# Kernel tuning notes

Hardware: AMD Instinct MI355X
Metric: run time of the kernel (lower is better)

Reference implementation:

```python
import jax, jax.numpy as jnp
import numpy as np

KERNEL_SIZE = (3, 3)
STRIDE = 1
PADDING = 'valid'  # 'valid' -> no padding; 'same' -> pad per module's pad_tensor


def setup_inputs() -> dict:
    key = jax.random.key(0)
    kx, kk = jax.random.split(key)
    C_in, H, W = 16, 2048, 2048
    C_out = 16
    hf, wf = KERNEL_SIZE
    x = jax.random.normal(kx, (C_in, H, W), dtype=jnp.float32)
    kernels = jax.random.normal(kk, (C_out, C_in, hf, wf), dtype=jnp.float32)
    return {"x": x, "kernels": kernels}


def _conv(x, kernels):
    # x: (C,H,W); kernels: (C_out,C_in,hf,wf)
    # The torch module's im2col + mm is exactly a cross-correlation (no kernel
    # flip), i.e., standard conv in DL convention.
    if PADDING == 'same':
        hf, wf = KERNEL_SIZE
        ph, pw = (hf - 1) // 2, (wf - 1) // 2
        # NOTE: original ConstantPad3d((0,0,pad_h,pad_h,pad_w,pad_w)) pads H by
        # pad_h and C by pad_w on a (C,H,W) tensor; for square kernels with
        # hf==wf the intended symmetric spatial pad is equivalent here.
        x = jnp.pad(x, ((0, 0), (ph, ph), (pw, pw)))
    out = jax.lax.conv_general_dilated(
        x[None],                      # (1,C,H,W)
        kernels,                      # (O,I,hf,wf)
        window_strides=(STRIDE, STRIDE),
        padding='VALID',
        dimension_numbers=('NCHW', 'OIHW', 'NCHW'),
    )
    return out[0]                     # (C_out,H_out,W_out)


def reference(x, kernels):
    return _conv(x, kernels)
```

## Files before the change

kernel.cpp:

```cpp
#include <hip/hip_runtime.h>


#define HIN   2048
#define WIN   2048
#define HOUT  2046
#define WOUT  2046
#define PLANE_IN  (HIN * WIN)
#define PLANE_OUT (HOUT * WOUT)
#define TR 34
#define TC 36
#define NTASK (TR * 18 * 2)
#define WF_U32 (5 * 64 * 4)

typedef __attribute__((ext_vector_type(8))) short bf16x8;
typedef __attribute__((ext_vector_type(4))) float f32x4;
typedef __attribute__((ext_vector_type(4))) unsigned u32x4;
typedef f32x4 __attribute__((aligned(4))) f32x4_u;

static __device__ __forceinline__ short f2bf(float f) {
    unsigned u = __float_as_uint(f);
    return (short)((u + 0x7FFFu + ((u >> 16) & 1u)) >> 16);
}
static __device__ __forceinline__ unsigned pk2(float lo, float hi) {
    unsigned a = __float_as_uint(lo);
    unsigned b = __float_as_uint(hi);
    a = (a + 0x7FFFu + ((a >> 16) & 1u)) >> 16;
    b = (b + 0x7FFFu + ((b >> 16) & 1u)) & 0xFFFF0000u;
    return a | b;
}

__global__ __launch_bounds__(64)
void wf_setup(const float* __restrict__ k, unsigned* __restrict__ wfbuf) {
    int lane = threadIdx.x;
    int m = lane & 15, g = lane >> 4;
    #pragma unroll
    for (int i = 0; i < 5; ++i) {
        u32x4 q;
        #pragma unroll
        for (int jj = 0; jj < 4; ++jj) {
            unsigned r = 0;
            #pragma unroll
            for (int e = 0; e < 2; ++e) {
                int kk  = 32 * i + 8 * g + 2 * jj + e;
                int tap = kk >> 4;
                int ci  = kk & 15;
                unsigned v = 0;
                if (tap < 9) v = (unsigned short)f2bf(k[(m * 16 + ci) * 9 + tap]);
                r |= v << (16 * e);
            }
            q[jj] = r;
        }
        *(u32x4*)(wfbuf + (i * 64 + lane) * 4) = q;
    }
}

__global__ __launch_bounds__(512, 6)
void conv3x3_fused(const float* __restrict__ x,
                   const unsigned* __restrict__ wfbuf,
                   float* __restrict__ out) {
    __shared__ unsigned lds[TR * TC * 8];

    const int tid  = threadIdx.x;
    const int lane = tid & 63;
    const int wv   = tid >> 6;
    const int m    = lane & 15;
    const int g    = lane >> 4;

    int bid = blockIdx.x;
    int swz = (bid & 7) * 512 + (bid >> 3);
    int h0 = (swz >> 6) * 32; if (h0 > HOUT - 32) h0 = HOUT - 32;
    int w0 = (swz & 63) * 32;

    #pragma unroll
    for (int p = 0; p < 3; ++p) {
        int t = p * 512 + tid;
        if (t < NTASK) {
            int wp  = t % 18;
            int r2  = t / 18;
            int cih = r2 & 1;
            int row = r2 >> 1;
            int c   = 2 * wp;
            int w   = w0 + c; if (w > WIN - 2) w = WIN - 2;
            const float* gp = x + (size_t)(cih * 8) * PLANE_IN
                                + (size_t)(h0 + row) * WIN + w;
            float2 f0 = *(const float2*)(gp + 0 * PLANE_IN);
            float2 f1 = *(const float2*)(gp + 1 * PLANE_IN);
            float2 f2 = *(const float2*)(gp + 2 * PLANE_IN);
            float2 f3 = *(const float2*)(gp + 3 * PLANE_IN);
            float2 f4 = *(const float2*)(gp + 4 * PLANE_IN);
            float2 f5 = *(const float2*)(gp + 5 * PLANE_IN);
            float2 f6 = *(const float2*)(gp + 6 * PLANE_IN);
            float2 f7 = *(const float2*)(gp + 7 * PLANE_IN);
            u32x4 ch0, ch1;
            ch0[0] = pk2(f0.x, f1.x); ch0[1] = pk2(f2.x, f3.x);
            ch0[2] = pk2(f4.x, f5.x); ch0[3] = pk2(f6.x, f7.x);
            ch1[0] = pk2(f0.y, f1.y); ch1[1] = pk2(f2.y, f3.y);
            ch1[2] = pk2(f4.y, f5.y); ch1[3] = pk2(f6.y, f7.y);
            int a = (((row * TC + c) * 32) + cih * 16) ^ ((c & 4) << 2);
            *(u32x4*)((char*)lds + a)      = ch0;
            *(u32x4*)((char*)lds + a + 32) = ch1;
        }
    }

    bf16x8 wf[5];
    #pragma unroll
    for (int i = 0; i < 5; ++i)
        wf[i] = *(const bf16x8*)(wfbuf + (i * 64 + lane) * 4);

    int off[5];
    #pragma unroll
    for (int i = 0; i < 5; ++i) {
        int tap = 2 * i + (g >> 1);
        if (tap > 8) tap = 8;
        int kh = tap / 3;
        int kw = tap - kh * 3;
        int col = m + kw;
        int o = (kh * TC + col) * 32 + (g & 1) * 16;
        off[i] = o ^ ((col & 4) << 2);
    }

    __syncthreads();

    const char* ldsb = (const char*)lds;

    #pragma unroll
    for (int hl4 = 0; hl4 < 4; ++hl4) {
        int hl = wv * 4 + hl4;
        int h  = h0 + hl;
        #pragma unroll
        for (int nh = 0; nh < 2; ++nh) {
            int wl = nh * 16;
            int tb = (hl * TC + wl) * 32;
            f32x4 acc = {0.f, 0.f, 0.f, 0.f};
            #pragma unroll
            for (int i = 0; i < 5; ++i) {
                bf16x8 a = *(const bf16x8*)(ldsb + (tb + off[i]));
                acc = __builtin_amdgcn_mfma_f32_16x16x32_bf16(a, wf[i], acc, 0, 0, 0);
            }
            int w = w0 + wl + g * 4;
            float* op = out + m * (size_t)PLANE_OUT + (size_t)h * WOUT + w;
            if (w + 3 < WOUT) {
                *(f32x4_u*)op = acc;
            } else {
                #pragma unroll
                for (int r = 0; r < 4; ++r)
                    if (w + r < WOUT) op[r] = acc[r];
            }
        }
    }
}

__global__ __launch_bounds__(256, 4)
void conv3x3_mfma(const float* __restrict__ x,
                  const float* __restrict__ k,
                  float* __restrict__ out) {
    __shared__ short lds[TR * 34 * 16];
    const int tid  = threadIdx.x;
    const int lane = tid & 63;
    const int wv   = tid >> 6;
    const int m    = lane & 15;
    const int g    = lane >> 4;
    int bid = blockIdx.x;
    int swz = (bid & 7) * 512 + (bid >> 3);
    int h0 = (swz >> 6) * 32;
    int w0 = (swz & 63) * 32;
    for (int p = tid; p < TR * 34; p += 256) {
        int r = p / 34, c = p - r * 34;
        int hh = h0 + r; if (hh > HIN - 1) hh = HIN - 1;
        int ww = w0 + c; if (ww > WIN - 1) ww = WIN - 1;
        const float* gp = x + hh * WIN + ww;
        short t[16];
        #pragma unroll
        for (int ci = 0; ci < 16; ++ci) t[ci] = f2bf(gp[ci * PLANE_IN]);
        bf16x8 lo, hi;
        #pragma unroll
        for (int j = 0; j < 8; ++j) { lo[j] = t[j]; hi[j] = t[8 + j]; }
        int sw = (c >> 2) & 1;
        bf16x8* dst = (bf16x8*)&lds[p * 16];
        dst[sw] = lo; dst[1 - sw] = hi;
    }
    bf16x8 wf[5];
    #pragma unroll
    for (int i = 0; i < 5; ++i)
        #pragma unroll
        for (int j = 0; j < 8; ++j) {
            int kk = 32 * i + 8 * g + j;
            int tap = kk >> 4, ci = kk & 15;
            short v = 0;
            if (tap < 9) v = f2bf(k[(m * 16 + ci) * 9 + tap]);
            wf[i][j] = v;
        }
    int off[5];
    #pragma unroll
    for (int i = 0; i < 5; ++i) {
        int tap = 2 * i + (g >> 1);
        if (tap > 8) tap = 8;
        int kh = tap / 3, kw = tap - kh * 3;
        int col = m + kw;
        int o = (kh * 34 + col) * 32 + (g & 1) * 16;
        off[i] = o ^ ((col & 4) << 2);
    }
    __syncthreads();
    const char* ldsb = (const char*)lds;
    const int coBase = g * 4;
    for (int hl8 = 0; hl8 < 8; ++hl8) {
        int hl = wv * 8 + hl8;
        int h = h0 + hl;
        bool hok = (h < HOUT);
        #pragma unroll
        for (int nh = 0; nh < 2; ++nh) {
            int wl = nh * 16;
            int tb = (hl * 34 + wl) * 32;
            f32x4 acc = {0.f, 0.f, 0.f, 0.f};
            #pragma unroll
            for (int i = 0; i < 5; ++i) {
                bf16x8 b = *(const bf16x8*)(ldsb + (tb + off[i]));
                acc = __builtin_amdgcn_mfma_f32_16x16x32_bf16(wf[i], b, acc, 0, 0, 0);
            }
            int w = w0 + wl + m;
            if (hok && w < WOUT) {
                float* op = out + h * WOUT + w;
                #pragma unroll
                for (int r = 0; r < 4; ++r)
                    op[(coBase + r) * PLANE_OUT] = acc[r];
            }
        }
    }
}

extern "C" void kernel_launch(void* const* d_in, const int* in_sizes, int n_in,
                              void* d_out, int out_size, void* d_ws, size_t ws_size,
                              hipStream_t stream) {
    const float* x = (const float*)d_in[0];
    const float* k = (const float*)d_in[1];
    float* out = (float*)d_out;
    if (ws_size >= WF_U32 * 4) {
        unsigned* wfbuf = (unsigned*)d_ws;
        wf_setup<<<dim3(1), dim3(64), 0, stream>>>(k, wfbuf);
        conv3x3_fused<<<dim3(4096), dim3(512), 0, stream>>>(x, wfbuf, out);
    } else {
        conv3x3_mfma<<<dim3(4096), dim3(256), 0, stream>>>(x, k, out);
    }
}
```

Measured before the change: 156.6 us.

## Use 1024-thread blocks with single-pass dwordx4 tile loads via inline asm

The fused conv kernel now launches 1024 threads per block, so 612 threads each load four columns across eight channels with global_load_dwordx4. The whole input tile arrives in one pass instead of three float2 passes. Each wave now computes two output rows instead of four. The goal is wider, fully issued global loads and more waves to hide latency. Inline asm with an explicit vmcnt(0) wait and a sched barrier stops the compiler from overlapping these loads with other work, and the launch bounds drop to 2 blocks per CU.

```diff
diff --git a/kernel.cpp b/kernel.cpp
--- a/kernel.cpp
+++ b/kernel.cpp
@@ -9,7 +9,7 @@
 #define PLANE_OUT (HOUT * WOUT)
 #define TR 34
 #define TC 36
-#define NTASK (TR * 18 * 2)
+#define NQTASK (TR * 9 * 2)
 #define WF_U32 (5 * 64 * 4)
 
 typedef __attribute__((ext_vector_type(8))) short bf16x8;
@@ -54,10 +54,13 @@
     }
 }
 
-__global__ __launch_bounds__(512, 6)
-void conv3x3_fused(const float* __restrict__ x,
-                   const unsigned* __restrict__ wfbuf,
-                   float* __restrict__ out) {
+#define GLOADX4(DST, ADDR) \
+    asm volatile("global_load_dwordx4 %0, %1, off" : "=&v"(DST) : "v"(ADDR))
+
+__global__ __launch_bounds__(1024, 2)
+void conv3x3_fused1k(const float* __restrict__ x,
+                     const unsigned* __restrict__ wfbuf,
+                     float* __restrict__ out) {
     __shared__ unsigned lds[TR * TC * 8];
 
     const int tid  = threadIdx.x;
@@ -71,35 +74,42 @@
     int h0 = (swz >> 6) * 32; if (h0 > HOUT - 32) h0 = HOUT - 32;
     int w0 = (swz & 63) * 32;
 
-    #pragma unroll
-    for (int p = 0; p < 3; ++p) {
-        int t = p * 512 + tid;
-        if (t < NTASK) {
-            int wp  = t % 18;
-            int r2  = t / 18;
-            int cih = r2 & 1;
-            int row = r2 >> 1;
-            int c   = 2 * wp;
-            int w   = w0 + c; if (w > WIN - 2) w = WIN - 2;
-            const float* gp = x + (size_t)(cih * 8) * PLANE_IN
-                                + (size_t)(h0 + row) * WIN + w;
-            float2 f0 = *(const float2*)(gp + 0 * PLANE_IN);
-            float2 f1 = *(const float2*)(gp + 1 * PLANE_IN);
-            float2 f2 = *(const float2*)(gp + 2 * PLANE_IN);
-            float2 f3 = *(const float2*)(gp + 3 * PLANE_IN);
-            float2 f4 = *(const float2*)(gp + 4 * PLANE_IN);
-            float2 f5 = *(const float2*)(gp + 5 * PLANE_IN);
-            float2 f6 = *(const float2*)(gp + 6 * PLANE_IN);
-            float2 f7 = *(const float2*)(gp + 7 * PLANE_IN);
-            u32x4 ch0, ch1;
-            ch0[0] = pk2(f0.x, f1.x); ch0[1] = pk2(f2.x, f3.x);
-            ch0[2] = pk2(f4.x, f5.x); ch0[3] = pk2(f6.x, f7.x);
-            ch1[0] = pk2(f0.y, f1.y); ch1[1] = pk2(f2.y, f3.y);
-            ch1[2] = pk2(f4.y, f5.y); ch1[3] = pk2(f6.y, f7.y);
-            int a = (((row * TC + c) * 32) + cih * 16) ^ ((c & 4) << 2);
-            *(u32x4*)((char*)lds + a)      = ch0;
-            *(u32x4*)((char*)lds + a + 32) = ch1;
-        }
+    if (tid < NQTASK) {
+        int t   = tid;
+        int q   = t % 9;
+        int r2  = t / 9;
+        int cih = r2 & 1;
+        int row = r2 >> 1;
+        int c   = 4 * q;
+        int w   = w0 + c; if (w > WIN - 4) w = WIN - 4;
+        const float* gp = x + (size_t)(cih * 8) * PLANE_IN
+                            + (size_t)(h0 + row) * WIN + w;
+        f32x4 f0, f1, f2, f3, f4, f5, f6, f7;
+        GLOADX4(f0, gp + 0 * (size_t)PLANE_IN);
+        GLOADX4(f1, gp + 1 * (size_t)PLANE_IN);
+        GLOADX4(f2, gp + 2 * (size_t)PLANE_IN);
+        GLOADX4(f3, gp + 3 * (size_t)PLANE_IN);
+        GLOADX4(f4, gp + 4 * (size_t)PLANE_IN);
+        GLOADX4(f5, gp + 5 * (size_t)PLANE_IN);
+        GLOADX4(f6, gp + 6 * (size_t)PLANE_IN);
+        GLOADX4(f7, gp + 7 * (size_t)PLANE_IN);
+        asm volatile("s_waitcnt vmcnt(0)" ::: "memory");
+        __builtin_amdgcn_sched_barrier(0);
+
+        int a = ((row * TC + c) * 32 + cih * 16) ^ ((c & 4) << 2);
+        u32x4 ch;
+        ch[0] = pk2(f0[0], f1[0]); ch[1] = pk2(f2[0], f3[0]);
+        ch[2] = pk2(f4[0], f5[0]); ch[3] = pk2(f6[0], f7[0]);
+        *(u32x4*)((char*)lds + a)      = ch;
+        ch[0] = pk2(f0[1], f1[1]); ch[1] = pk2(f2[1], f3[1]);
+        ch[2] = pk2(f4[1], f5[1]); ch[3] = pk2(f6[1], f7[1]);
+        *(u32x4*)((char*)lds + a + 32) = ch;
+        ch[0] = pk2(f0[2], f1[2]); ch[1] = pk2(f2[2], f3[2]);
+        ch[2] = pk2(f4[2], f5[2]); ch[3] = pk2(f6[2], f7[2]);
+        *(u32x4*)((char*)lds + a + 64) = ch;
+        ch[0] = pk2(f0[3], f1[3]); ch[1] = pk2(f2[3], f3[3]);
+        ch[2] = pk2(f4[3], f5[3]); ch[3] = pk2(f6[3], f7[3]);
+        *(u32x4*)((char*)lds + a + 96) = ch;
     }
 
     bf16x8 wf[5];
@@ -124,8 +134,8 @@
     const char* ldsb = (const char*)lds;
 
     #pragma unroll
-    for (int hl4 = 0; hl4 < 4; ++hl4) {
-        int hl = wv * 4 + hl4;
+    for (int hl2 = 0; hl2 < 2; ++hl2) {
+        int hl = wv * 2 + hl2;
         int h  = h0 + hl;
         #pragma unroll
         for (int nh = 0; nh < 2; ++nh) {
@@ -154,7 +164,7 @@
 void conv3x3_mfma(const float* __restrict__ x,
                   const float* __restrict__ k,
                   float* __restrict__ out) {
-    __shared__ short lds[TR * 34 * 16];
+    __shared__ short lds2[TR * 34 * 16];
     const int tid  = threadIdx.x;
     const int lane = tid & 63;
     const int wv   = tid >> 6;
@@ -176,7 +186,7 @@
         #pragma unroll
         for (int j = 0; j < 8; ++j) { lo[j] = t[j]; hi[j] = t[8 + j]; }
         int sw = (c >> 2) & 1;
-        bf16x8* dst = (bf16x8*)&lds[p * 16];
+        bf16x8* dst = (bf16x8*)&lds2[p * 16];
         dst[sw] = lo; dst[1 - sw] = hi;
     }
     bf16x8 wf[5];
@@ -201,7 +211,7 @@
         off[i] = o ^ ((col & 4) << 2);
     }
     __syncthreads();
-    const char* ldsb = (const char*)lds;
+    const char* ldsb = (const char*)lds2;
     const int coBase = g * 4;
     for (int hl8 = 0; hl8 < 8; ++hl8) {
         int hl = wv * 8 + hl8;
@@ -237,7 +247,7 @@
     if (ws_size >= WF_U32 * 4) {
         unsigned* wfbuf = (unsigned*)d_ws;
         wf_setup<<<dim3(1), dim3(64), 0, stream>>>(k, wfbuf);
-        conv3x3_fused<<<dim3(4096), dim3(512), 0, stream>>>(x, wfbuf, out);
+        conv3x3_fused1k<<<dim3(4096), dim3(1024), 0, stream>>>(x, wfbuf, out);
     } else {
         conv3x3_mfma<<<dim3(4096), dim3(256), 0, stream>>>(x, k, out);
     }
```

Result: faster. 152.6 us (-2.6%).
